# Performance work log

Measured on AMD Instinct MI355X. Metric: run time of the kernel, lower is better.

The kernel has to match this reference:

```python
import jax, jax.numpy as jnp
import numpy as np

N_NODES = 100000
N_EDGES = 1600000
D_IN = 128
D_HID = 128
D_OUT = 128


def _sage_conv(x, src, dst, W_l, b_l, W_r, num_nodes):
    # PyG SAGEConv (aggr='mean'): out = lin_l(mean_{j in N(i)} x_j) + lin_r(x_i)
    msg = x[src]  # [E, d] gather source features
    agg = jax.ops.segment_sum(msg, dst, num_segments=num_nodes)  # [N, d]
    deg = jax.ops.segment_sum(jnp.ones((src.shape[0],), x.dtype), dst, num_segments=num_nodes)
    mean = agg / jnp.maximum(deg, 1.0)[:, None]
    return mean @ W_l.T + b_l + x @ W_r.T


def setup_inputs() -> dict:
    key = jax.random.key(0)
    ks = jax.random.split(key, 8)
    x = jax.random.normal(ks[0], (N_NODES, D_IN), dtype=jnp.float32)
    edge_index = jax.random.randint(ks[1], (2, N_EDGES), 0, N_NODES, dtype=jnp.int64)
    s = 1.0 / np.sqrt(D_IN)
    W_l1 = jax.random.uniform(ks[2], (D_HID, D_IN), jnp.float32, -s, s)
    b_l1 = jnp.zeros((D_HID,), jnp.float32)
    W_r1 = jax.random.uniform(ks[3], (D_HID, D_IN), jnp.float32, -s, s)
    s2 = 1.0 / np.sqrt(D_HID)
    W_l2 = jax.random.uniform(ks[4], (D_OUT, D_HID), jnp.float32, -s2, s2)
    b_l2 = jnp.zeros((D_OUT,), jnp.float32)
    W_r2 = jax.random.uniform(ks[5], (D_OUT, D_HID), jnp.float32, -s2, s2)
    return {"x": x, "edge_index": edge_index, "W_l1": W_l1, "b_l1": b_l1,
            "W_r1": W_r1, "W_l2": W_l2, "b_l2": b_l2, "W_r2": W_r2}


def reference(x, edge_index, W_l1, b_l1, W_r1, W_l2, b_l2, W_r2):
    src, dst = edge_index[0], edge_index[1]
    n = x.shape[0]
    h = _sage_conv(x, src, dst, W_l1, b_l1, W_r1, n)
    h = jax.nn.relu(h)
    out = _sage_conv(h, src, dst, W_l2, b_l2, W_r2, n)
    return out
```

## Files before the change

kernel.cpp:

```cpp
#include <hip/hip_runtime.h>
#include <stdint.h>

typedef short bf16x8 __attribute__((ext_vector_type(8)));
typedef unsigned short u16x8 __attribute__((ext_vector_type(8)));
typedef float f32x4 __attribute__((ext_vector_type(4)));

#define NPB 512
#define BSHIFT 9
#define MAXBUCK 256
#define STAGE_CAP 12288
#define LROW 136

__device__ __forceinline__ short f2bf(float f) {
    uint32_t u = __float_as_uint(f);
    u += 0x7fffu + ((u >> 16) & 1u);
    return (short)(u >> 16);
}
__device__ __forceinline__ float bf2f(unsigned short s) {
    return __uint_as_float((uint32_t)s << 16);
}

__global__ __launch_bounds__(256) void convx_kernel(const float* __restrict__ in,
                                                    short* __restrict__ out, int n) {
    int i = (blockIdx.x * 256 + threadIdx.x) * 8;
    if (i + 8 <= n) {
        const float4 v0 = *(const float4*)(in + i);
        const float4 v1 = *(const float4*)(in + i + 4);
        bf16x8 o;
        o[0] = f2bf(v0.x); o[1] = f2bf(v0.y); o[2] = f2bf(v0.z); o[3] = f2bf(v0.w);
        o[4] = f2bf(v1.x); o[5] = f2bf(v1.y); o[6] = f2bf(v1.z); o[7] = f2bf(v1.w);
        *(bf16x8*)(out + i) = o;
    } else {
        for (int j = i; j < n; ++j) out[j] = f2bf(in[j]);
    }
}

__global__ void convw4_kernel(const float* __restrict__ w0, const float* __restrict__ w1,
                              const float* __restrict__ w2, const float* __restrict__ w3,
                              short* __restrict__ o0, short* __restrict__ o1,
                              short* __restrict__ o2, short* __restrict__ o3) {
    int i = blockIdx.x * 256 + threadIdx.x;
    o0[i] = f2bf(w0[i]);
    o1[i] = f2bf(w1[i]);
    o2[i] = f2bf(w2[i]);
    o3[i] = f2bf(w3[i]);
}

__global__ __launch_bounds__(256) void bhist_kernel(const int* __restrict__ dst,
                                                    int* __restrict__ bcnt, int E, int B) {
    __shared__ int h[MAXBUCK];
    for (int i = threadIdx.x; i < B; i += 256) h[i] = 0;
    __syncthreads();
    int stride = gridDim.x * 256;
    for (int e = blockIdx.x * 256 + threadIdx.x; e < E; e += stride)
        atomicAdd(&h[dst[e] >> BSHIFT], 1);
    __syncthreads();
    for (int i = threadIdx.x; i < B; i += 256)
        if (h[i]) atomicAdd(&bcnt[i], h[i]);
}

__global__ __launch_bounds__(256) void bscan_kernel(const int* __restrict__ bcnt,
                                                    int* __restrict__ bbase,
                                                    int* __restrict__ gcur,
                                                    int* __restrict__ rowptr,
                                                    int E, int N, int B) {
    __shared__ int s[256];
    int t = threadIdx.x;
    int v = (t < B) ? bcnt[t] : 0;
    s[t] = v;
    __syncthreads();
    for (int off = 1; off < 256; off <<= 1) {
        int a = (t >= off) ? s[t - off] : 0;
        __syncthreads();
        s[t] += a;
        __syncthreads();
    }
    int excl = s[t] - v;
    if (t < B) { bbase[t] = excl; gcur[t] = excl; }
    if (t == B - 1) bbase[B] = excl + v;
    if (t == 0) rowptr[N] = E;
}

__global__ __launch_bounds__(256) void bin_kernel(const int* __restrict__ src,
                                                  const int* __restrict__ dst,
                                                  int* __restrict__ gcur,
                                                  unsigned int* __restrict__ binned,
                                                  int E, int B) {
    __shared__ int cnt[MAXBUCK];
    __shared__ int base[MAXBUCK];
    for (int i = threadIdx.x; i < B; i += 256) cnt[i] = 0;
    __syncthreads();
    const int e0 = blockIdx.x * 4096;
    const int eEnd = (e0 + 4096 < E) ? (e0 + 4096) : E;
#pragma unroll 4
    for (int e = e0 + threadIdx.x; e < eEnd; e += 256)
        atomicAdd(&cnt[dst[e] >> BSHIFT], 1);
    __syncthreads();
    for (int i = threadIdx.x; i < B; i += 256) {
        int c = cnt[i];
        base[i] = c ? atomicAdd(&gcur[i], c) : 0;
        cnt[i] = 0;
    }
    __syncthreads();
#pragma unroll 4
    for (int e = e0 + threadIdx.x; e < eEnd; e += 256) {
        int sv = src[e], dv = dst[e];
        int b = dv >> BSHIFT;
        int off = atomicAdd(&cnt[b], 1);
        binned[base[b] + off] = ((unsigned)sv << BSHIFT) | (unsigned)(dv & (NPB - 1));
    }
}

__global__ __launch_bounds__(256) void build_kernel(const unsigned int* __restrict__ binned,
                                                    const int* __restrict__ bbase,
                                                    int* __restrict__ rowptr,
                                                    int* __restrict__ csr, int N) {
    __shared__ int hist[NPB];
    __shared__ int cur[NPB];
    __shared__ int scanb[256];
    __shared__ int stage[STAGE_CAP];
    const int b = blockIdx.x;
    const int t = threadIdx.x;
    const int cbeg = bbase[b], cend = bbase[b + 1];
    const int cnt = cend - cbeg;
    for (int i = t; i < NPB; i += 256) hist[i] = 0;
    __syncthreads();
    for (int i = t; i < cnt; i += 256)
        atomicAdd(&hist[binned[cbeg + i] & (NPB - 1)], 1);
    __syncthreads();
    const int h0 = hist[2 * t], h1 = hist[2 * t + 1];
    const int ps = h0 + h1;
    scanb[t] = ps;
    __syncthreads();
    for (int off = 1; off < 256; off <<= 1) {
        int a = (t >= off) ? scanb[t - off] : 0;
        __syncthreads();
        scanb[t] += a;
        __syncthreads();
    }
    const int e0 = scanb[t] - ps;
    cur[2 * t]     = e0;
    cur[2 * t + 1] = e0 + h0;
    __syncthreads();
    const int node0 = b << BSHIFT;
    for (int i = t; i < NPB; i += 256) {
        int node = node0 + i;
        if (node < N) rowptr[node] = cbeg + cur[i];
    }
    __syncthreads();
    for (int i = t; i < cnt; i += 256) {
        unsigned rec = binned[cbeg + i];
        int ld  = rec & (NPB - 1);
        int pos = atomicAdd(&cur[ld], 1);
        if (pos < STAGE_CAP) stage[pos] = (int)(rec >> BSHIFT);
        else                 csr[cbeg + pos] = (int)(rec >> BSHIFT);
    }
    __syncthreads();
    const int lim = cnt < STAGE_CAP ? cnt : STAGE_CAP;
    for (int i = t; i < lim; i += 256)
        csr[cbeg + i] = stage[i];
}

#define ACC8(u) do { \
    a0 += bf2f(u[0]); a1 += bf2f(u[1]); a2 += bf2f(u[2]); a3 += bf2f(u[3]); \
    a4 += bf2f(u[4]); a5 += bf2f(u[5]); a6 += bf2f(u[6]); a7 += bf2f(u[7]); } while (0)

template <bool RELU>
__global__ __launch_bounds__(256) void fused_kernel(
    const short* __restrict__ feat, const int* __restrict__ csr,
    const int* __restrict__ rowptr,
    const short* __restrict__ Wl, const short* __restrict__ Wr,
    const float* __restrict__ bias,
    short* __restrict__ outb, float* __restrict__ outf, int N)
{
    __shared__ short lmean[64 * LROW];
    const int lane = threadIdx.x & 63;
    const int wave = threadIdx.x >> 6;
    const int q    = lane >> 4;
    const int ql   = lane & 15;
    const int m0   = blockIdx.x * 64 + wave * 16;

    for (int it = 0; it < 4; ++it) {
        const int node = m0 + it * 4 + q;
        float a0=0,a1=0,a2=0,a3=0,a4=0,a5=0,a6=0,a7=0;
        if (node < N) {
            const int beg = rowptr[node], end = rowptr[node + 1];
            int e = beg;
            for (; e + 8 <= end; e += 8) {
                const int s0 = csr[e],   s1 = csr[e+1], s2 = csr[e+2], s3 = csr[e+3];
                const int s4 = csr[e+4], s5 = csr[e+5], s6 = csr[e+6], s7 = csr[e+7];
                const u16x8 u0 = *(const u16x8*)(feat + (size_t)s0 * 128 + ql * 8);
                const u16x8 u1 = *(const u16x8*)(feat + (size_t)s1 * 128 + ql * 8);
                const u16x8 u2 = *(const u16x8*)(feat + (size_t)s2 * 128 + ql * 8);
                const u16x8 u3 = *(const u16x8*)(feat + (size_t)s3 * 128 + ql * 8);
                const u16x8 u4 = *(const u16x8*)(feat + (size_t)s4 * 128 + ql * 8);
                const u16x8 u5 = *(const u16x8*)(feat + (size_t)s5 * 128 + ql * 8);
                const u16x8 u6 = *(const u16x8*)(feat + (size_t)s6 * 128 + ql * 8);
                const u16x8 u7 = *(const u16x8*)(feat + (size_t)s7 * 128 + ql * 8);
                ACC8(u0); ACC8(u1); ACC8(u2); ACC8(u3);
                ACC8(u4); ACC8(u5); ACC8(u6); ACC8(u7);
            }
            if (e + 4 <= end) {
                const int s0 = csr[e], s1 = csr[e+1], s2 = csr[e+2], s3 = csr[e+3];
                const u16x8 u0 = *(const u16x8*)(feat + (size_t)s0 * 128 + ql * 8);
                const u16x8 u1 = *(const u16x8*)(feat + (size_t)s1 * 128 + ql * 8);
                const u16x8 u2 = *(const u16x8*)(feat + (size_t)s2 * 128 + ql * 8);
                const u16x8 u3 = *(const u16x8*)(feat + (size_t)s3 * 128 + ql * 8);
                ACC8(u0); ACC8(u1); ACC8(u2); ACC8(u3);
                e += 4;
            }
            for (; e < end; ++e) {
                const u16x8 u = *(const u16x8*)(feat + (size_t)csr[e] * 128 + ql * 8);
                ACC8(u);
            }
            const float r = 1.0f / fmaxf((float)(end - beg), 1.0f);
            bf16x8 o;
            o[0] = f2bf(a0 * r); o[1] = f2bf(a1 * r); o[2] = f2bf(a2 * r); o[3] = f2bf(a3 * r);
            o[4] = f2bf(a4 * r); o[5] = f2bf(a5 * r); o[6] = f2bf(a6 * r); o[7] = f2bf(a7 * r);
            *(bf16x8*)(lmean + (size_t)(wave * 16 + it * 4 + q) * LROW + ql * 8) = o;
        }
    }

    f32x4 acc[8];
#pragma unroll
    for (int i = 0; i < 8; ++i) acc[i] = (f32x4)0.0f;
    const bool valid = (m0 + ql < N);

#pragma unroll
    for (int kk = 0; kk < 4; ++kk) {
        const int kb = kk * 32 + q * 8;
        const bf16x8 a = *(const bf16x8*)(lmean + (size_t)(wave * 16 + ql) * LROW + kb);
#pragma unroll
        for (int nt = 0; nt < 8; ++nt) {
            const bf16x8 b = *(const bf16x8*)(Wl + (size_t)(nt * 16 + ql) * 128 + kb);
            acc[nt] = __builtin_amdgcn_mfma_f32_16x16x32_bf16(a, b, acc[nt], 0, 0, 0);
        }
    }
#pragma unroll
    for (int kk = 0; kk < 4; ++kk) {
        const int kb = kk * 32 + q * 8;
        bf16x8 a = (bf16x8)0;
        if (valid) a = *(const bf16x8*)(feat + (size_t)(m0 + ql) * 128 + kb);
#pragma unroll
        for (int nt = 0; nt < 8; ++nt) {
            const bf16x8 b = *(const bf16x8*)(Wr + (size_t)(nt * 16 + ql) * 128 + kb);
            acc[nt] = __builtin_amdgcn_mfma_f32_16x16x32_bf16(a, b, acc[nt], 0, 0, 0);
        }
    }

    const int rbase = m0 + q * 4;
#pragma unroll
    for (int nt = 0; nt < 8; ++nt) {
        const int col = nt * 16 + ql;
        const float bc = bias[col];
#pragma unroll
        for (int r = 0; r < 4; ++r) {
            const int node = rbase + r;
            if (node < N) {
                float v = acc[nt][r] + bc;
                if (RELU) outb[(size_t)node * 128 + col] = f2bf(fmaxf(v, 0.0f));
                else      outf[(size_t)node * 128 + col] = v;
            }
        }
    }
}

extern "C" void kernel_launch(void* const* d_in, const int* in_sizes, int n_in,
                              void* d_out, int out_size, void* d_ws, size_t ws_size,
                              hipStream_t stream) {
    const float* x   = (const float*)d_in[0];
    const int*   ei  = (const int*)d_in[1];
    const float* Wl1 = (const float*)d_in[2];
    const float* bl1 = (const float*)d_in[3];
    const float* Wr1 = (const float*)d_in[4];
    const float* Wl2 = (const float*)d_in[5];
    const float* bl2 = (const float*)d_in[6];
    const float* Wr2 = (const float*)d_in[7];

    const int N = in_sizes[0] / 128;
    const int E = in_sizes[1] / 2;
    const int* src = ei;
    const int* dst = ei + E;
    const int B = (N + NPB - 1) >> BSHIFT;

    char* wsb = (char*)d_ws;
    short* hbuf = (short*)wsb;
    size_t off = (size_t)N * 128 * 2;
    short* wl1 = (short*)(wsb + off); off += 16384 * 2;
    short* wr1 = (short*)(wsb + off); off += 16384 * 2;
    short* wl2 = (short*)(wsb + off); off += 16384 * 2;
    short* wr2 = (short*)(wsb + off); off += 16384 * 2;
    int* rowptr = (int*)(wsb + off);
    off += ((size_t)(N + 1) * 4 + 15) & ~(size_t)15;
    int* csr = (int*)(wsb + off);
    off += ((size_t)E * 4 + 15) & ~(size_t)15;
    unsigned int* binned = (unsigned int*)(wsb + off);
    off += ((size_t)E * 4 + 15) & ~(size_t)15;
    int* bcnt  = (int*)(wsb + off);
    int* bbase = bcnt + (MAXBUCK + 1);
    int* gcur  = bbase + (MAXBUCK + 1);

    short* xb  = (short*)d_out;
    float* out = (float*)d_out;

    const int fusedBlocks = (N + 63) / 64;
    const int binBlocks   = (E + 4095) / 4096;

    convx_kernel<<<(N * 128 / 8 + 255) / 256, 256, 0, stream>>>(x, xb, N * 128);
    convw4_kernel<<<64, 256, 0, stream>>>(Wl1, Wr1, Wl2, Wr2, wl1, wr1, wl2, wr2);

    (void)hipMemsetAsync(bcnt, 0, (size_t)(MAXBUCK + 1) * sizeof(int), stream);
    bhist_kernel<<<512, 256, 0, stream>>>(dst, bcnt, E, B);
    bscan_kernel<<<1, 256, 0, stream>>>(bcnt, bbase, gcur, rowptr, E, N, B);
    bin_kernel<<<binBlocks, 256, 0, stream>>>(src, dst, gcur, binned, E, B);
    build_kernel<<<B, 256, 0, stream>>>(binned, bbase, rowptr, csr, N);

    fused_kernel<true><<<fusedBlocks, 256, 0, stream>>>(xb, csr, rowptr, wl1, wr1, bl1,
                                                        hbuf, (float*)nullptr, N);
    fused_kernel<false><<<fusedBlocks, 256, 0, stream>>>(hbuf, csr, rowptr, wl2, wr2, bl2,
                                                         (short*)nullptr, out, N);
}
```

Baseline: 454.2 us.

## Build CSR via per-node histogram and atomic scatter; shrink fused blocks

Replaces the two-level bucket binning plus LDS-staged build with a per-node degree histogram (fused into one prep kernel with the bf16 conversions), a two-level scan, and a direct global-atomic scatter into CSR. The fused aggregation kernel now uses 128-thread blocks covering 32 nodes, drops the 8-wide gather unroll in favour of 4-wide, and zero-fills out-of-range rows. The aim is fewer launches and passes over the edge list, at the cost of many contended global atomics and a CSR order within each row that is no longer deterministic.

```diff
diff --git a/kernel.cpp b/kernel.cpp
--- a/kernel.cpp
+++ b/kernel.cpp
@@ -7,8 +7,6 @@
 
 #define NPB 512
 #define BSHIFT 9
-#define MAXBUCK 256
-#define STAGE_CAP 12288
 #define LROW 136
 
 __device__ __forceinline__ short f2bf(float f) {
@@ -20,53 +18,77 @@
     return __uint_as_float((uint32_t)s << 16);
 }
 
-__global__ __launch_bounds__(256) void convx_kernel(const float* __restrict__ in,
-                                                    short* __restrict__ out, int n) {
-    int i = (blockIdx.x * 256 + threadIdx.x) * 8;
-    if (i + 8 <= n) {
-        const float4 v0 = *(const float4*)(in + i);
-        const float4 v1 = *(const float4*)(in + i + 4);
-        bf16x8 o;
-        o[0] = f2bf(v0.x); o[1] = f2bf(v0.y); o[2] = f2bf(v0.z); o[3] = f2bf(v0.w);
-        o[4] = f2bf(v1.x); o[5] = f2bf(v1.y); o[6] = f2bf(v1.z); o[7] = f2bf(v1.w);
-        *(bf16x8*)(out + i) = o;
-    } else {
-        for (int j = i; j < n; ++j) out[j] = f2bf(in[j]);
-    }
-}
-
-__global__ void convw4_kernel(const float* __restrict__ w0, const float* __restrict__ w1,
-                              const float* __restrict__ w2, const float* __restrict__ w3,
-                              short* __restrict__ o0, short* __restrict__ o1,
-                              short* __restrict__ o2, short* __restrict__ o3) {
-    int i = blockIdx.x * 256 + threadIdx.x;
-    o0[i] = f2bf(w0[i]);
-    o1[i] = f2bf(w1[i]);
-    o2[i] = f2bf(w2[i]);
-    o3[i] = f2bf(w3[i]);
-}
-
-__global__ __launch_bounds__(256) void bhist_kernel(const int* __restrict__ dst,
-                                                    int* __restrict__ bcnt, int E, int B) {
-    __shared__ int h[MAXBUCK];
-    for (int i = threadIdx.x; i < B; i += 256) h[i] = 0;
+__global__ __launch_bounds__(256) void prep_kernel(
+    const float* __restrict__ x, short* __restrict__ xb, int nx,
+    const float* __restrict__ w0, const float* __restrict__ w1,
+    const float* __restrict__ w2, const float* __restrict__ w3,
+    short* __restrict__ o0, short* __restrict__ o1,
+    short* __restrict__ o2, short* __restrict__ o3,
+    const int* __restrict__ dst, int* __restrict__ cnt, int E,
+    int cxBlocks, int histBlocks)
+{
+    int b = blockIdx.x;
+    if (b < cxBlocks) {
+        int i = (b * 256 + threadIdx.x) * 8;
+        if (i + 8 <= nx) {
+            const float4 v0 = *(const float4*)(x + i);
+            const float4 v1 = *(const float4*)(x + i + 4);
+            bf16x8 o;
+            o[0] = f2bf(v0.x); o[1] = f2bf(v0.y); o[2] = f2bf(v0.z); o[3] = f2bf(v0.w);
+            o[4] = f2bf(v1.x); o[5] = f2bf(v1.y); o[6] = f2bf(v1.z); o[7] = f2bf(v1.w);
+            *(bf16x8*)(xb + i) = o;
+        } else {
+            for (int j = i; j < nx; ++j) xb[j] = f2bf(x[j]);
+        }
+        return;
+    }
+    b -= cxBlocks;
+    if (b < 64) {
+        int i = b * 256 + threadIdx.x;
+        o0[i] = f2bf(w0[i]);
+        o1[i] = f2bf(w1[i]);
+        o2[i] = f2bf(w2[i]);
+        o3[i] = f2bf(w3[i]);
+        return;
+    }
+    b -= 64;
+    const int stride = histBlocks * 256;
+    for (int e = b * 256 + threadIdx.x; e < E; e += stride)
+        atomicAdd(&cnt[dst[e]], 1);
+}
+
+__global__ __launch_bounds__(256) void scan512_kernel(const int* __restrict__ cnt,
+                                                      int* __restrict__ rowptr,
+                                                      int* __restrict__ bsum, int N) {
+    __shared__ int scanb[256];
+    const int b = blockIdx.x;
+    const int t = threadIdx.x;
+    const int base = b << BSHIFT;
+    const int v0 = cnt[base + 2 * t];
+    const int v1 = cnt[base + 2 * t + 1];
+    const int ps = v0 + v1;
+    scanb[t] = ps;
     __syncthreads();
-    int stride = gridDim.x * 256;
-    for (int e = blockIdx.x * 256 + threadIdx.x; e < E; e += stride)
-        atomicAdd(&h[dst[e] >> BSHIFT], 1);
-    __syncthreads();
-    for (int i = threadIdx.x; i < B; i += 256)
-        if (h[i]) atomicAdd(&bcnt[i], h[i]);
-}
-
-__global__ __launch_bounds__(256) void bscan_kernel(const int* __restrict__ bcnt,
-                                                    int* __restrict__ bbase,
-                                                    int* __restrict__ gcur,
-                                                    int* __restrict__ rowptr,
-                                                    int E, int N, int B) {
+    for (int off = 1; off < 256; off <<= 1) {
+        int a = (t >= off) ? scanb[t - off] : 0;
+        __syncthreads();
+        scanb[t] += a;
+        __syncthreads();
+    }
+    const int e0 = scanb[t] - ps;
+    const int n0 = base + 2 * t;
+    if (n0 < N)     rowptr[n0]     = e0;
+    if (n0 + 1 < N) rowptr[n0 + 1] = e0 + v0;
+    if (t == 255) bsum[b] = scanb[255];
+}
+
+__global__ __launch_bounds__(256) void topscan_kernel(const int* __restrict__ bsum,
+                                                      int* __restrict__ bbase,
+                                                      int* __restrict__ rowptr,
+                                                      int E, int N, int B) {
     __shared__ int s[256];
     int t = threadIdx.x;
-    int v = (t < B) ? bcnt[t] : 0;
+    int v = (t < B) ? bsum[t] : 0;
     s[t] = v;
     __syncthreads();
     for (int off = 1; off < 256; off <<= 1) {
@@ -75,90 +97,33 @@
         s[t] += a;
         __syncthreads();
     }
-    int excl = s[t] - v;
-    if (t < B) { bbase[t] = excl; gcur[t] = excl; }
-    if (t == B - 1) bbase[B] = excl + v;
+    if (t < B) bbase[t] = s[t] - v;
     if (t == 0) rowptr[N] = E;
 }
 
-__global__ __launch_bounds__(256) void bin_kernel(const int* __restrict__ src,
-                                                  const int* __restrict__ dst,
-                                                  int* __restrict__ gcur,
-                                                  unsigned int* __restrict__ binned,
-                                                  int E, int B) {
-    __shared__ int cnt[MAXBUCK];
-    __shared__ int base[MAXBUCK];
-    for (int i = threadIdx.x; i < B; i += 256) cnt[i] = 0;
-    __syncthreads();
-    const int e0 = blockIdx.x * 4096;
-    const int eEnd = (e0 + 4096 < E) ? (e0 + 4096) : E;
-#pragma unroll 4
-    for (int e = e0 + threadIdx.x; e < eEnd; e += 256)
-        atomicAdd(&cnt[dst[e] >> BSHIFT], 1);
-    __syncthreads();
-    for (int i = threadIdx.x; i < B; i += 256) {
-        int c = cnt[i];
-        base[i] = c ? atomicAdd(&gcur[i], c) : 0;
-        cnt[i] = 0;
-    }
-    __syncthreads();
-#pragma unroll 4
-    for (int e = e0 + threadIdx.x; e < eEnd; e += 256) {
-        int sv = src[e], dv = dst[e];
-        int b = dv >> BSHIFT;
-        int off = atomicAdd(&cnt[b], 1);
-        binned[base[b] + off] = ((unsigned)sv << BSHIFT) | (unsigned)(dv & (NPB - 1));
-    }
-}
-
-__global__ __launch_bounds__(256) void build_kernel(const unsigned int* __restrict__ binned,
+__global__ __launch_bounds__(256) void apply_kernel(int* __restrict__ rowptr,
                                                     const int* __restrict__ bbase,
-                                                    int* __restrict__ rowptr,
-                                                    int* __restrict__ csr, int N) {
-    __shared__ int hist[NPB];
-    __shared__ int cur[NPB];
-    __shared__ int scanb[256];
-    __shared__ int stage[STAGE_CAP];
-    const int b = blockIdx.x;
-    const int t = threadIdx.x;
-    const int cbeg = bbase[b], cend = bbase[b + 1];
-    const int cnt = cend - cbeg;
-    for (int i = t; i < NPB; i += 256) hist[i] = 0;
-    __syncthreads();
-    for (int i = t; i < cnt; i += 256)
-        atomicAdd(&hist[binned[cbeg + i] & (NPB - 1)], 1);
-    __syncthreads();
-    const int h0 = hist[2 * t], h1 = hist[2 * t + 1];
-    const int ps = h0 + h1;
-    scanb[t] = ps;
-    __syncthreads();
-    for (int off = 1; off < 256; off <<= 1) {
-        int a = (t >= off) ? scanb[t - off] : 0;
-        __syncthreads();
-        scanb[t] += a;
-        __syncthreads();
-    }
-    const int e0 = scanb[t] - ps;
-    cur[2 * t]     = e0;
-    cur[2 * t + 1] = e0 + h0;
-    __syncthreads();
-    const int node0 = b << BSHIFT;
-    for (int i = t; i < NPB; i += 256) {
-        int node = node0 + i;
-        if (node < N) rowptr[node] = cbeg + cur[i];
-    }
-    __syncthreads();
-    for (int i = t; i < cnt; i += 256) {
-        unsigned rec = binned[cbeg + i];
-        int ld  = rec & (NPB - 1);
-        int pos = atomicAdd(&cur[ld], 1);
-        if (pos < STAGE_CAP) stage[pos] = (int)(rec >> BSHIFT);
-        else                 csr[cbeg + pos] = (int)(rec >> BSHIFT);
-    }
-    __syncthreads();
-    const int lim = cnt < STAGE_CAP ? cnt : STAGE_CAP;
-    for (int i = t; i < lim; i += 256)
-        csr[cbeg + i] = stage[i];
+                                                    int* __restrict__ gcur, int N) {
+    int node = blockIdx.x * 256 + threadIdx.x;
+    if (node < N) {
+        int r = rowptr[node] + bbase[node >> BSHIFT];
+        rowptr[node] = r;
+        gcur[node] = r;
+    }
+}
+
+__global__ __launch_bounds__(256) void scatter_kernel(const int* __restrict__ src,
+                                                      const int* __restrict__ dst,
+                                                      int* __restrict__ gcur,
+                                                      int* __restrict__ csr,
+                                                      int E, int nBlocks) {
+    const int stride = nBlocks * 256;
+    for (int e = blockIdx.x * 256 + threadIdx.x; e < E; e += stride) {
+        const int d = dst[e];
+        const int s = src[e];
+        const int p = atomicAdd(&gcur[d], 1);
+        csr[p] = s;
+    }
 }
 
 #define ACC8(u) do { \
@@ -166,48 +131,34 @@
     a4 += bf2f(u[4]); a5 += bf2f(u[5]); a6 += bf2f(u[6]); a7 += bf2f(u[7]); } while (0)
 
 template <bool RELU>
-__global__ __launch_bounds__(256) void fused_kernel(
+__global__ __launch_bounds__(128) void fused_kernel(
     const short* __restrict__ feat, const int* __restrict__ csr,
     const int* __restrict__ rowptr,
     const short* __restrict__ Wl, const short* __restrict__ Wr,
     const float* __restrict__ bias,
     short* __restrict__ outb, float* __restrict__ outf, int N)
 {
-    __shared__ short lmean[64 * LROW];
+    __shared__ short lmean[32 * LROW];
     const int lane = threadIdx.x & 63;
     const int wave = threadIdx.x >> 6;
     const int q    = lane >> 4;
     const int ql   = lane & 15;
-    const int m0   = blockIdx.x * 64 + wave * 16;
+    const int m0   = blockIdx.x * 32 + wave * 16;
 
     for (int it = 0; it < 4; ++it) {
         const int node = m0 + it * 4 + q;
+        const int lrow = wave * 16 + it * 4 + q;
         float a0=0,a1=0,a2=0,a3=0,a4=0,a5=0,a6=0,a7=0;
         if (node < N) {
             const int beg = rowptr[node], end = rowptr[node + 1];
             int e = beg;
-            for (; e + 8 <= end; e += 8) {
-                const int s0 = csr[e],   s1 = csr[e+1], s2 = csr[e+2], s3 = csr[e+3];
-                const int s4 = csr[e+4], s5 = csr[e+5], s6 = csr[e+6], s7 = csr[e+7];
-                const u16x8 u0 = *(const u16x8*)(feat + (size_t)s0 * 128 + ql * 8);
-                const u16x8 u1 = *(const u16x8*)(feat + (size_t)s1 * 128 + ql * 8);
-                const u16x8 u2 = *(const u16x8*)(feat + (size_t)s2 * 128 + ql * 8);
-                const u16x8 u3 = *(const u16x8*)(feat + (size_t)s3 * 128 + ql * 8);
-                const u16x8 u4 = *(const u16x8*)(feat + (size_t)s4 * 128 + ql * 8);
-                const u16x8 u5 = *(const u16x8*)(feat + (size_t)s5 * 128 + ql * 8);
-                const u16x8 u6 = *(const u16x8*)(feat + (size_t)s6 * 128 + ql * 8);
-                const u16x8 u7 = *(const u16x8*)(feat + (size_t)s7 * 128 + ql * 8);
-                ACC8(u0); ACC8(u1); ACC8(u2); ACC8(u3);
-                ACC8(u4); ACC8(u5); ACC8(u6); ACC8(u7);
-            }
-            if (e + 4 <= end) {
+            for (; e + 4 <= end; e += 4) {
                 const int s0 = csr[e], s1 = csr[e+1], s2 = csr[e+2], s3 = csr[e+3];
                 const u16x8 u0 = *(const u16x8*)(feat + (size_t)s0 * 128 + ql * 8);
                 const u16x8 u1 = *(const u16x8*)(feat + (size_t)s1 * 128 + ql * 8);
                 const u16x8 u2 = *(const u16x8*)(feat + (size_t)s2 * 128 + ql * 8);
                 const u16x8 u3 = *(const u16x8*)(feat + (size_t)s3 * 128 + ql * 8);
                 ACC8(u0); ACC8(u1); ACC8(u2); ACC8(u3);
-                e += 4;
             }
             for (; e < end; ++e) {
                 const u16x8 u = *(const u16x8*)(feat + (size_t)csr[e] * 128 + ql * 8);
@@ -217,7 +168,9 @@
             bf16x8 o;
             o[0] = f2bf(a0 * r); o[1] = f2bf(a1 * r); o[2] = f2bf(a2 * r); o[3] = f2bf(a3 * r);
             o[4] = f2bf(a4 * r); o[5] = f2bf(a5 * r); o[6] = f2bf(a6 * r); o[7] = f2bf(a7 * r);
-            *(bf16x8*)(lmean + (size_t)(wave * 16 + it * 4 + q) * LROW + ql * 8) = o;
+            *(bf16x8*)(lmean + (size_t)lrow * LROW + ql * 8) = o;
+        } else {
+            *(bf16x8*)(lmean + (size_t)lrow * LROW + ql * 8) = (bf16x8)0;
         }
     }
 
@@ -294,29 +247,34 @@
     off += ((size_t)(N + 1) * 4 + 15) & ~(size_t)15;
     int* csr = (int*)(wsb + off);
     off += ((size_t)E * 4 + 15) & ~(size_t)15;
-    unsigned int* binned = (unsigned int*)(wsb + off);
-    off += ((size_t)E * 4 + 15) & ~(size_t)15;
-    int* bcnt  = (int*)(wsb + off);
-    int* bbase = bcnt + (MAXBUCK + 1);
-    int* gcur  = bbase + (MAXBUCK + 1);
+    int* cnt = (int*)(wsb + off);
+    off += ((size_t)B * NPB * 4 + 15) & ~(size_t)15;
+    int* gcur = (int*)(wsb + off);
+    off += ((size_t)N * 4 + 15) & ~(size_t)15;
+    int* bsum  = (int*)(wsb + off);
+    int* bbase = bsum + 256;
 
     short* xb  = (short*)d_out;
     float* out = (float*)d_out;
 
-    const int fusedBlocks = (N + 63) / 64;
-    const int binBlocks   = (E + 4095) / 4096;
-
-    convx_kernel<<<(N * 128 / 8 + 255) / 256, 256, 0, stream>>>(x, xb, N * 128);
-    convw4_kernel<<<64, 256, 0, stream>>>(Wl1, Wr1, Wl2, Wr2, wl1, wr1, wl2, wr2);
-
-    (void)hipMemsetAsync(bcnt, 0, (size_t)(MAXBUCK + 1) * sizeof(int), stream);
-    bhist_kernel<<<512, 256, 0, stream>>>(dst, bcnt, E, B);
-    bscan_kernel<<<1, 256, 0, stream>>>(bcnt, bbase, gcur, rowptr, E, N, B);
-    bin_kernel<<<binBlocks, 256, 0, stream>>>(src, dst, gcur, binned, E, B);
-    build_kernel<<<B, 256, 0, stream>>>(binned, bbase, rowptr, csr, N);
-
-    fused_kernel<true><<<fusedBlocks, 256, 0, stream>>>(xb, csr, rowptr, wl1, wr1, bl1,
+    const int nx = N * 128;
+    const int cxBlocks   = (nx / 8 + 255) / 256;
+    const int histBlocks = 1024;
+    const int scatBlocks = 1024;
+    const int fusedBlocks = (N + 31) / 32;
+
+    (void)hipMemsetAsync(cnt, 0, (size_t)B * NPB * sizeof(int), stream);
+
+    prep_kernel<<<cxBlocks + 64 + histBlocks, 256, 0, stream>>>(
+        x, xb, nx, Wl1, Wr1, Wl2, Wr2, wl1, wr1, wl2, wr2,
+        dst, cnt, E, cxBlocks, histBlocks);
+    scan512_kernel<<<B, 256, 0, stream>>>(cnt, rowptr, bsum, N);
+    topscan_kernel<<<1, 256, 0, stream>>>(bsum, bbase, rowptr, E, N, B);
+    apply_kernel<<<(N + 255) / 256, 256, 0, stream>>>(rowptr, bbase, gcur, N);
+    scatter_kernel<<<scatBlocks, 256, 0, stream>>>(src, dst, gcur, csr, E, scatBlocks);
+
+    fused_kernel<true><<<fusedBlocks, 128, 0, stream>>>(xb, csr, rowptr, wl1, wr1, bl1,
                                                         hbuf, (float*)nullptr, N);
-    fused_kernel<false><<<fusedBlocks, 256, 0, stream>>>(hbuf, csr, rowptr, wl2, wr2, bl2,
+    fused_kernel<false><<<fusedBlocks, 128, 0, stream>>>(hbuf, csr, rowptr, wl2, wr2, bl2,
                                                          (short*)nullptr, out, N);
 }
```

Measured after the change: 563.3 us. +24.0%, slower.
